# Optimization experiments

Measured on AMD Instinct MI355X. Metric: run time of the kernel, lower is better.

The kernel has to match this reference:

```python
import jax, jax.numpy as jnp
from jax import lax
import numpy as np

NEG = jnp.float32(-1e9)


def monotonic_alignment_search(logp, text_lengths, mel_lengths):
    """Glow-TTS style MAS. logp: [B, Tt, Tm] (log_softmax over text axis).
    Returns integer durations [B, Tt] summing to mel_lengths per batch."""
    B, Tt, Tm = logp.shape
    i_range = jnp.arange(Tt)
    text_mask = i_range[None, :] < text_lengths[:, None]            # [B, Tt]
    logp = jnp.where(text_mask[:, :, None], logp, NEG)

    # ---- forward DP over mel frames: Q[i,j] = logp[i,j] + max(Q[i,j-1], Q[i-1,j-1])
    q0 = jnp.where(i_range[None, :] == 0, logp[:, :, 0], NEG)        # [B, Tt]

    def fwd(q, lp_j):
        q_shift = jnp.concatenate([jnp.full((B, 1), NEG), q[:, :-1]], axis=1)
        take_diag = q_shift > q                                      # came from i-1
        q_new = lp_j + jnp.maximum(q, q_shift)
        return q_new, take_diag

    _, choices = lax.scan(fwd, q0, jnp.moveaxis(logp[:, :, 1:], 2, 0))  # [Tm-1, B, Tt]
    choices = jnp.concatenate([jnp.zeros((1, B, Tt), bool), choices], axis=0)  # align j

    # ---- backtrack from (text_len-1, mel_len-1) down to j=0
    b_idx = jnp.arange(B)

    def bwd(i, j):
        active = j < mel_lengths                                     # [B]
        dur_inc = (active[:, None] & (i_range[None, :] == i[:, None]))
        ch = choices[j, b_idx, i]                                    # [B] bool
        i_new = jnp.where(active & (j > 0), i - ch.astype(i.dtype), i)
        return i_new, dur_inc

    i0 = text_lengths - 1
    _, durs = lax.scan(bwd, i0, jnp.arange(Tm - 1, -1, -1))
    return durs.sum(0).astype(jnp.int32)                             # [B, Tt]


def length_regulate(h_text, durations, mel_lengths, Tm):
    """Expand h_text [B,Tt,D] by durations [B,Tt] to [B,Tm,D]."""
    B, Tt, D = h_text.shape
    cum = jnp.cumsum(durations, axis=1)                              # [B, Tt]
    j = jnp.arange(Tm)
    idx = (cum[:, None, :] <= j[None, :, None]).sum(-1)              # [B, Tm]
    idx = jnp.clip(idx, 0, Tt - 1)
    h_exp = jnp.take_along_axis(h_text, idx[:, :, None], axis=1)     # [B, Tm, D]
    mel_mask = j[None, :] < mel_lengths[:, None]
    return h_exp * mel_mask[:, :, None].astype(h_exp.dtype)


def setup_inputs() -> dict:
    B, Tt, Tm, D, M = 32, 512, 2048, 512, 80
    k = jax.random.split(jax.random.key(0), 6)
    return {
        "h_text": jax.random.normal(k[0], (B, Tt, D), jnp.float32),
        "mel": jax.random.normal(k[1], (B, M, Tm), jnp.float32),
        "text_lengths": jax.random.randint(k[2], (B,), 256, Tt + 1, jnp.int32),
        "mel_lengths": jax.random.randint(k[3], (B,), 1024, Tm + 1, jnp.int32),
        "w_proj": jax.random.normal(k[4], (D, M), jnp.float32) * 0.02,
        "b_proj": jnp.zeros((D,), jnp.float32),
        "log_dur_pred": jax.random.normal(k[5], (B, Tt), jnp.float32) * 0.5,
    }


def reference(h_text, mel, text_lengths, mel_lengths, w_proj, b_proj, log_dur_pred):
    B, Tt, D = h_text.shape
    Tm = mel.shape[2]

    # mel_proj = Linear(n_mels -> d_model) on mel.transpose(1,2)
    mel_proj = jnp.einsum('bmt,dm->btd', mel, w_proj) + b_proj       # [B, Tm, D]

    # alignment scores + masked log_softmax over text axis
    attn = jnp.einsum('btd,bsd->bts', h_text, mel_proj)              # [B, Tt, Tm]
    text_mask = jnp.arange(Tt)[None, :] >= text_lengths[:, None]
    mel_mask = jnp.arange(Tm)[None, :] >= mel_lengths[:, None]
    attn = jnp.where(text_mask[:, :, None], NEG, attn)
    attn = jnp.where(mel_mask[:, None, :], NEG, attn)
    logp = jax.nn.log_softmax(attn, axis=1)

    durations = monotonic_alignment_search(logp, text_lengths, mel_lengths)

    # duration loss (masked sum-MSE in log domain)
    dur_mask = (jnp.arange(Tt)[None, :] < text_lengths[:, None]).astype(jnp.float32)
    log_dur_gt = jnp.log(jnp.clip(durations.astype(jnp.float32), 1.0, None))
    diff = log_dur_pred * dur_mask - log_dur_gt * dur_mask
    dur_loss = jnp.sum(diff * diff) / jnp.sum(dur_mask)

    h_expanded = length_regulate(h_text, durations, mel_lengths, Tm)  # [B, Tm, D]
    return (h_expanded, dur_loss, durations)
```

## Files before the change

### kernel.cpp

```cpp
#include <hip/hip_runtime.h>
#include <math.h>

#define Bn 32
#define TT 512
#define TM 2048
#define DD 512
#define MMp 80
#define NEGF (-1.0e9f)

constexpr size_t LOSS_OFF = (size_t)Bn * TM * DD;
constexpr size_t DUR_OFF  = LOSS_OFF + 1;

__global__ __launch_bounds__(256) void k0_wtx(const float* __restrict__ w,
                                              const float* __restrict__ bias,
                                              float* __restrict__ wTx) {
    int m = blockIdx.x;
    for (int d = threadIdx.x; d < DD; d += 256) {
        float v = 0.f;
        if (m < 80) v = w[d * 80 + m];
        else if (m == 80) v = bias[d];
        wTx[m * DD + d] = v;
    }
}

__global__ __launch_bounds__(256) void k1_hw(const float* __restrict__ h_text,
                                             const float* __restrict__ wTx,
                                             float* __restrict__ hwX) {
    int bid = blockIdx.x;
    int b = bid >> 3;
    int i0 = (bid & 7) * 64;
    int t = threadIdx.x;
    int tr = t & 15, tc = t >> 4;
    __shared__ __align__(16) float Asub[64 * 68];
    __shared__ __align__(16) float Bsub[96 * 68];
    float acc[4][6];
#pragma unroll
    for (int a = 0; a < 4; ++a)
#pragma unroll
        for (int c = 0; c < 6; ++c) acc[a][c] = 0.f;

    for (int d0 = 0; d0 < DD; d0 += 64) {
        __syncthreads();
#pragma unroll
        for (int p = 0; p < 4; ++p) {
            int lin = p * 256 + t;
            int r = lin >> 4, dq = lin & 15;
            *(float4*)&Asub[r * 68 + dq * 4] =
                *(const float4*)&h_text[((size_t)(b * TT + i0 + r)) * DD + d0 + dq * 4];
        }
#pragma unroll
        for (int p = 0; p < 6; ++p) {
            int lin = p * 256 + t;
            int cc = lin >> 4, dq = lin & 15;
            *(float4*)&Bsub[cc * 68 + dq * 4] =
                *(const float4*)&wTx[(size_t)cc * DD + d0 + dq * 4];
        }
        __syncthreads();
#pragma unroll
        for (int dd = 0; dd < 16; ++dd) {
            float4 a[4], bb[6];
#pragma unroll
            for (int ri = 0; ri < 4; ++ri)
                a[ri] = *(const float4*)&Asub[(tr * 4 + ri) * 68 + dd * 4];
#pragma unroll
            for (int ci = 0; ci < 6; ++ci)
                bb[ci] = *(const float4*)&Bsub[(tc * 6 + ci) * 68 + dd * 4];
#pragma unroll
            for (int ri = 0; ri < 4; ++ri)
#pragma unroll
                for (int ci = 0; ci < 6; ++ci) {
                    acc[ri][ci] += a[ri].x * bb[ci].x;
                    acc[ri][ci] += a[ri].y * bb[ci].y;
                    acc[ri][ci] += a[ri].z * bb[ci].z;
                    acc[ri][ci] += a[ri].w * bb[ci].w;
                }
        }
    }
#pragma unroll
    for (int ri = 0; ri < 4; ++ri)
#pragma unroll
        for (int ci = 0; ci < 6; ++ci)
            hwX[((size_t)b * 96 + tc * 6 + ci) * DD + i0 + tr * 4 + ri] = acc[ri][ci];
}

__global__ __launch_bounds__(256) void k2_attn(const float* __restrict__ hwX,
                                               const float* __restrict__ mel,
                                               const int* __restrict__ tlen,
                                               const int* __restrict__ mlen,
                                               float* __restrict__ logpT) {
    const int b = blockIdx.y;
    const int ml = mlen[b];
    const int j0 = blockIdx.x * 32;
    if (j0 >= ml) return;
    const int tl = tlen[b];
    const int tid = threadIdx.x;
    const int ig = tid >> 2;
    const int jg = tid & 3;

    __shared__ __align__(16) float hwS[16 * 512];
    __shared__ __align__(16) float melS[16 * 32];
    __shared__ float red[32 * 64];
    __shared__ float colmax[32];
    __shared__ float lsum[32];

    float acc[8][8];
#pragma unroll
    for (int a = 0; a < 8; ++a)
#pragma unroll
        for (int c = 0; c < 8; ++c) acc[a][c] = 0.f;

    for (int mc = 0; mc < 80; mc += 16) {
        __syncthreads();
#pragma unroll
        for (int p = 0; p < 8; ++p) {
            int lin = p * 256 + tid;
            int mm = lin >> 7, iq = lin & 127;
            *(float4*)&hwS[mm * 512 + iq * 4] =
                *(const float4*)&hwX[((size_t)b * 96 + mc + mm) * DD + iq * 4];
        }
#pragma unroll
        for (int p = 0; p < 2; ++p) {
            int lin = p * 256 + tid;
            int mm = lin >> 5, jj = lin & 31;
            melS[lin] = mel[((size_t)b * 80 + mc + mm) * TM + j0 + jj];
        }
        __syncthreads();
#pragma unroll
        for (int mm = 0; mm < 16; ++mm) {
            float4 a0 = *(const float4*)&hwS[mm * 512 + ig * 8];
            float4 a1 = *(const float4*)&hwS[mm * 512 + ig * 8 + 4];
            float4 b0 = *(const float4*)&melS[mm * 32 + jg * 8];
            float4 b1 = *(const float4*)&melS[mm * 32 + jg * 8 + 4];
            float av[8] = {a0.x, a0.y, a0.z, a0.w, a1.x, a1.y, a1.z, a1.w};
            float bv[8] = {b0.x, b0.y, b0.z, b0.w, b1.x, b1.y, b1.z, b1.w};
#pragma unroll
            for (int ii = 0; ii < 8; ++ii)
#pragma unroll
                for (int jj = 0; jj < 8; ++jj) acc[ii][jj] += av[ii] * bv[jj];
        }
    }
    float4 h0 = *(const float4*)&hwX[((size_t)b * 96 + 80) * DD + ig * 8];
    float4 h1 = *(const float4*)&hwX[((size_t)b * 96 + 80) * DD + ig * 8 + 4];
    float hb[8] = {h0.x, h0.y, h0.z, h0.w, h1.x, h1.y, h1.z, h1.w};
#pragma unroll
    for (int ii = 0; ii < 8; ++ii) {
        bool valid = (ig * 8 + ii) < tl;
#pragma unroll
        for (int jj = 0; jj < 8; ++jj)
            acc[ii][jj] = valid ? (acc[ii][jj] + hb[ii]) : NEGF;
    }
    __syncthreads();
#pragma unroll
    for (int jj = 0; jj < 8; ++jj) {
        float m = acc[0][jj];
#pragma unroll
        for (int ii = 1; ii < 8; ++ii) m = fmaxf(m, acc[ii][jj]);
        red[(jg * 8 + jj) * 64 + ig] = m;
    }
    __syncthreads();
    if (tid < 32) {
        float m = red[tid * 64];
        for (int g = 1; g < 64; ++g) m = fmaxf(m, red[tid * 64 + g]);
        colmax[tid] = m;
    }
    __syncthreads();
#pragma unroll
    for (int jj = 0; jj < 8; ++jj) {
        float cm = colmax[jg * 8 + jj];
        float s = 0.f;
#pragma unroll
        for (int ii = 0; ii < 8; ++ii) s += expf(acc[ii][jj] - cm);
        red[(jg * 8 + jj) * 64 + ig] = s;
    }
    __syncthreads();
    if (tid < 32) {
        float s = 0.f;
        for (int g = 0; g < 64; ++g) s += red[tid * 64 + g];
        lsum[tid] = logf(s);
    }
    __syncthreads();
#pragma unroll
    for (int jj = 0; jj < 8; ++jj) {
        int j = j0 + jg * 8 + jj;
        if (j < ml) {
            float cm = colmax[jg * 8 + jj], ls = lsum[jg * 8 + jj];
            float o[8];
#pragma unroll
            for (int ii = 0; ii < 8; ++ii) {
                int i = ig * 8 + ii;
                o[ii] = (i < tl) ? ((acc[ii][jj] - cm) - ls) : NEGF;
            }
            float* dst = &logpT[((size_t)b * TM + j) * TT + ig * 8];
            *(float4*)dst = make_float4(o[0], o[1], o[2], o[3]);
            *(float4*)(dst + 4) = make_float4(o[4], o[5], o[6], o[7]);
        }
    }
}

#define KVB 16
#define NKB 128

typedef float vf4 __attribute__((ext_vector_type(4)));

__device__ __forceinline__ void lds_dma16(const float* g, float* l) {
    __builtin_amdgcn_global_load_lds((const __attribute__((address_space(1))) void*)g,
                                     (__attribute__((address_space(3))) void*)l,
                                     16, 0, 0);
}

#define SB0() __builtin_amdgcn_sched_barrier(0)

__device__ __forceinline__ float dpp_shr1(float old, float src) {
    return __int_as_float(__builtin_amdgcn_update_dpp(
        __float_as_int(old), __float_as_int(src), 0x138, 0xF, 0xF, false));
}
__device__ __forceinline__ float dpp_ror1(float src) {
    return __int_as_float(__builtin_amdgcn_update_dpp(
        __float_as_int(src), __float_as_int(src), 0x13C, 0xF, 0xF, false));
}

__global__ __launch_bounds__(64, 1) void k3_dp(const float* __restrict__ logpT,
                                               const int* __restrict__ tlen,
                                               const int* __restrict__ mlen,
                                               unsigned* __restrict__ gwords,
                                               int* __restrict__ idxmap,
                                               float* __restrict__ dOut) {
    const int b = blockIdx.x;
    const int lane = threadIdx.x;
    const int tl = tlen[b];
    const int ml = mlen[b];

    __shared__ __align__(16) float ring[2][KVB][512];
    __shared__ int durs[TT];
    for (int idx = lane; idx < TT; idx += 64) durs[idx] = 0;

    const float* colbase = logpT + (size_t)b * TM * TT;
    unsigned* gwb = gwords + (size_t)b * TT * 64;

    float qa[4], qb[4];
    unsigned accA[4], accB[4];
#pragma unroll
    for (int k = 0; k < 4; ++k) { qa[k] = NEGF; qb[k] = NEGF; accA[k] = 0u; accB[k] = 0u; }
    float q00 = colbase[0];
    asm volatile("" :: "v"(q00));
    if (lane == 0) qa[0] = q00;

    unsigned* gpA = gwb + (size_t)(4 * lane) * 64;
    unsigned* gpB = gwb + (size_t)(256 + 4 * lane) * 64;
    int woff = 0;
    int jj = 1;
    const int lane4 = lane * 4;

#define DMA_BATCH(nb_, slot_) do {                                             \
        const float* src_ = colbase + (size_t)(1 + (nb_) * KVB) * 512 + lane4; \
        float* dst_ = &ring[slot_][0][0];                                      \
        _Pragma("unroll")                                                      \
        for (int c_ = 0; c_ < KVB; ++c_) {                                     \
            lds_dma16(src_ + c_ * 512,       dst_ + c_ * 512);                 \
            lds_dma16(src_ + c_ * 512 + 256, dst_ + c_ * 512 + 256);           \
        }                                                                      \
    } while (0)

#define COL1(la_, lb_) do {                                                    \
        float wrap_ = dpp_ror1(qa[3]);                   \
        float nA0_ = dpp_shr1(NEGF, qa[3]);         \
        float nB0_ = dpp_shr1(wrap_, qb[3]);           \
        float nA_[4], nB_[4];                                                  \
        nA_[0] = nA0_; nB_[0] = nB0_;                                          \
        _Pragma("unroll")                                                      \
        for (int k_ = 1; k_ < 4; ++k_) { nA_[k_] = qa[k_ - 1]; nB_[k_] = qb[k_ - 1]; } \
        const unsigned m32_ = 1u << (jj & 31);                                 \
        _Pragma("unroll")                                                      \
        for (int k_ = 0; k_ < 4; ++k_) {                                       \
            if (nA_[k_] > qa[k_]) accA[k_] |= m32_;                            \
            qa[k_] = la_[k_] + fmaxf(qa[k_], nA_[k_]);                         \
            if (nB_[k_] > qb[k_]) accB[k_] |= m32_;                            \
            qb[k_] = lb_[k_] + fmaxf(qb[k_], nB_[k_]);                         \
        }                                                                      \
        if ((jj & 31) == 31) {                              \
            _Pragma("unroll")                                                  \
            for (int k_ = 0; k_ < 4; ++k_) {                                   \
                gpA[k_ * 64 + woff] = accA[k_]; accA[k_] = 0u;                 \
                gpB[k_ * 64 + woff] = accB[k_]; accB[k_] = 0u;                 \
            }                                                                  \
            ++woff;                                                            \
        }                                                                      \
        ++jj;                                                                  \
    } while (0)

#define READG(slab_, c0_, ga_, gb_) do {                                       \
        _Pragma("unroll")                                                      \
        for (int p_ = 0; p_ < 4; ++p_) {                                       \
            ga_[p_] = *(const vf4*)&slab_[(c0_ + p_) * 512 + lane4];           \
            gb_[p_] = *(const vf4*)&slab_[(c0_ + p_) * 512 + 256 + lane4];     \
        }                                                                      \
    } while (0)

#define COMPG(ga_, gb_) do {                                                   \
        _Pragma("unroll")                                                      \
        for (int p_ = 0; p_ < 4; ++p_) COL1(ga_[p_], gb_[p_]);                 \
    } while (0)

    DMA_BATCH(0, 0);
    DMA_BATCH(1, 1);

    for (int n = 0; n < NKB; ++n) {
        asm volatile("s_waitcnt vmcnt(32)" ::: "memory");
        SB0();
        const float* slab = &ring[n & 1][0][0];
        vf4 xA[4], xB[4], yA[4], yB[4];
        READG(slab, 0, xA, xB);
        READG(slab, 4, yA, yB);
        COMPG(xA, xB);
        READG(slab, 8, xA, xB);
        COMPG(yA, yB);
        READG(slab, 12, yA, yB);
        COMPG(xA, xB);
        COMPG(yA, yB);
        SB0();
        asm volatile("s_waitcnt lgkmcnt(0)" ::: "memory");
        SB0();
        if (n + 2 < NKB) DMA_BATCH(n + 2, n & 1);
        SB0();
    }
    asm volatile("s_waitcnt vmcnt(0) lgkmcnt(0)" ::: "memory");
#undef DMA_BATCH
#undef COL1
#undef READG
#undef COMPG

    __threadfence();
    __syncthreads();

    {
        int i = tl - 1;
        int j = ml - 1;
        unsigned r0, r1, r2, r3, r4, r5, r6, r7;
        {
            int a0 = tl - 1, a1 = tl - 2, a2 = tl - 3, a3 = tl - 4;
            int a4 = tl - 5, a5 = tl - 6, a6 = tl - 7, a7 = tl - 8;
            a1 = a1 < 0 ? 0 : a1; a2 = a2 < 0 ? 0 : a2; a3 = a3 < 0 ? 0 : a3;
            a4 = a4 < 0 ? 0 : a4; a5 = a5 < 0 ? 0 : a5; a6 = a6 < 0 ? 0 : a6;
            a7 = a7 < 0 ? 0 : a7;
            r0 = gwb[a0 * 64 + lane]; r1 = gwb[a1 * 64 + lane];
            r2 = gwb[a2 * 64 + lane]; r3 = gwb[a3 * 64 + lane];
            r4 = gwb[a4 * 64 + lane]; r5 = gwb[a5 * 64 + lane];
            r6 = gwb[a6 * 64 + lane]; r7 = gwb[a7 * 64 + lane];
        }
        int nf = tl - 9;
        int guard = TT + 2;
        while (guard-- > 0) {
            unsigned w = r0;
            r0 = r1; r1 = r2; r2 = r3; r3 = r4; r4 = r5; r5 = r6; r6 = r7;
            {
                int rf = (nf < 0) ? 0 : nf;
                r7 = gwb[rf * 64 + lane];
                --nf;
            }
            int jw = j >> 5, rr = j & 31;
            unsigned topmask = (rr == 31) ? 0xFFFFFFFFu : ((1u << (rr + 1)) - 1u);
            unsigned wm = (lane < jw) ? w : ((lane == jw) ? (w & topmask) : 0u);
            unsigned long long bal = __ballot(wm != 0u);
            if (bal == 0ull) {
                if (lane == 0) durs[i] = j + 1;
                break;
            }
            int hl = 63 - __clzll(bal);
            unsigned whl = (unsigned)__builtin_amdgcn_readlane((int)wm, hl);
            int jp = (hl << 5) + (31 - __clz(whl));
            if (lane == 0) durs[i] = j - jp + 1;
            j = jp - 1;
            if (--i < 0) break;
        }
    }
    __syncthreads();

    int d[8], pre[8];
    int run = 0;
#pragma unroll
    for (int k = 0; k < 8; ++k) { d[k] = durs[lane * 8 + k]; pre[k] = run; run += d[k]; }
    int v = run;
#pragma unroll
    for (int off = 1; off < 64; off <<= 1) {
        int n = __shfl_up(v, off);
        if (lane >= off) v += n;
    }
    int base = v - run;
#pragma unroll
    for (int k = 0; k < 8; ++k) {
        int i = lane * 8 + k;
        dOut[DUR_OFF + (size_t)b * TT + i] = (float)d[k];
        int st = base + pre[k];
        int en = st + d[k];
        if (en > TM) en = TM;
        if (st < 0) st = 0;
        for (int t2 = st; t2 < en; ++t2) idxmap[b * TM + t2] = i;
    }
}

__global__ __launch_bounds__(128) void k4_expand(const float* __restrict__ h_text,
                                                 const int* __restrict__ idxmap,
                                                 const int* __restrict__ mlen,
                                                 float* __restrict__ dOut) {
    int bid = blockIdx.x;
    int b = bid >> 11;
    int j = bid & (TM - 1);
    int t = threadIdx.x;
    float4* orow = (float4*)dOut + (size_t)bid * 128;
    if (j < mlen[b]) {
        int i = idxmap[bid] & (TT - 1);
        const float4* hrow = (const float4*)h_text + ((size_t)(b * TT + i)) * 128;
        orow[t] = hrow[t];
    } else {
        orow[t] = make_float4(0.f, 0.f, 0.f, 0.f);
    }
}

__global__ __launch_bounds__(256) void k5_loss(const float* __restrict__ pred,
                                               const int* __restrict__ tlen,
                                               float* __restrict__ dOut) {
    __shared__ float rs[256];
    __shared__ int rc[256];
    int t = threadIdx.x;
    float s = 0.f;
    int c = 0;
    for (int idx = t; idx < Bn * TT; idx += 256) {
        int b = idx >> 9, i = idx & 511;
        if (i < tlen[b]) {
            float dv = dOut[DUR_OFF + idx];
            float lg = logf(fmaxf(dv, 1.0f));
            float df = pred[idx] - lg;
            s += df * df;
            c += 1;
        }
    }
    rs[t] = s; rc[t] = c;
    __syncthreads();
    for (int off = 128; off > 0; off >>= 1) {
        if (t < off) { rs[t] += rs[t + off]; rc[t] += rc[t + off]; }
        __syncthreads();
    }
    if (t == 0) dOut[LOSS_OFF] = rs[0] / (float)rc[0];
}

extern "C" void kernel_launch(void* const* d_in, const int* in_sizes, int n_in,
                              void* d_out, int out_size, void* d_ws, size_t ws_size,
                              hipStream_t stream) {
    const float* h_text = (const float*)d_in[0];
    const float* mel    = (const float*)d_in[1];
    const int*   tlen   = (const int*)d_in[2];
    const int*   mlen   = (const int*)d_in[3];
    const float* w      = (const float*)d_in[4];
    const float* bias   = (const float*)d_in[5];
    const float* pred   = (const float*)d_in[6];
    float* out = (float*)d_out;

    float*    logpT  = (float*)d_ws;
    float*    hwX    = logpT + (size_t)Bn * TM * TT;
    float*    wTx    = hwX + (size_t)Bn * 96 * DD;
    unsigned* gwords = (unsigned*)(wTx + 96 * DD);
    int*      idxmap = (int*)(gwords + (size_t)Bn * TT * 64);

    k0_wtx<<<dim3(96), dim3(256), 0, stream>>>(w, bias, wTx);
    k1_hw<<<dim3(256), dim3(256), 0, stream>>>(h_text, wTx, hwX);
    k2_attn<<<dim3(64, 32), dim3(256), 0, stream>>>(hwX, mel, tlen, mlen, logpT);
    k3_dp<<<dim3(32), dim3(64), 0, stream>>>(logpT, tlen, mlen, gwords, idxmap, out);
    k4_expand<<<dim3(Bn * TM), dim3(128), 0, stream>>>(h_text, idxmap, mlen, out);
    k5_loss<<<dim3(1), dim3(256), 0, stream>>>(pred, tlen, out);
}
```

Baseline: 829.4 us.

## Split DP kernel into compute wave and eight producer DMA waves

The single-wave MAS forward DP kernel becomes a 576-thread block. Wave 0 runs the serial DP recurrence out of LDS, while eight producer waves each DMA two columns of the next 16-column batch into the other ring slot. Each batch ends with a __syncthreads instead of the old hand-tuned vmcnt waits. The aim is to take global-to-LDS load issue off the latency-critical DP wave, at the cost of a block barrier per batch and going from two batches of prefetch to one.

```diff
diff --git a/kernel.cpp b/kernel.cpp
--- a/kernel.cpp
+++ b/kernel.cpp
@@ -199,6 +199,7 @@
 
 #define KVB 16
 #define NKB 128
+#define K3T 576
 
 typedef float vf4 __attribute__((ext_vector_type(4)));
 
@@ -208,8 +209,6 @@
                                      16, 0, 0);
 }
 
-#define SB0() __builtin_amdgcn_sched_barrier(0)
-
 __device__ __forceinline__ float dpp_shr1(float old, float src) {
     return __int_as_float(__builtin_amdgcn_update_dpp(
         __float_as_int(old), __float_as_int(src), 0x138, 0xF, 0xF, false));
@@ -219,20 +218,22 @@
         __float_as_int(src), __float_as_int(src), 0x13C, 0xF, 0xF, false));
 }
 
-__global__ __launch_bounds__(64, 1) void k3_dp(const float* __restrict__ logpT,
-                                               const int* __restrict__ tlen,
-                                               const int* __restrict__ mlen,
-                                               unsigned* __restrict__ gwords,
-                                               int* __restrict__ idxmap,
-                                               float* __restrict__ dOut) {
+__global__ __launch_bounds__(K3T, 1) void k3_dp(const float* __restrict__ logpT,
+                                                const int* __restrict__ tlen,
+                                                const int* __restrict__ mlen,
+                                                unsigned* __restrict__ gwords,
+                                                int* __restrict__ idxmap,
+                                                float* __restrict__ dOut) {
     const int b = blockIdx.x;
-    const int lane = threadIdx.x;
+    const int tid = threadIdx.x;
+    const int wid = tid >> 6;
+    const int lane = tid & 63;
     const int tl = tlen[b];
     const int ml = mlen[b];
 
     __shared__ __align__(16) float ring[2][KVB][512];
     __shared__ int durs[TT];
-    for (int idx = lane; idx < TT; idx += 64) durs[idx] = 0;
+    for (int idx = tid; idx < TT; idx += K3T) durs[idx] = 0;
 
     const float* colbase = logpT + (size_t)b * TM * TT;
     unsigned* gwb = gwords + (size_t)b * TT * 64;
@@ -241,24 +242,23 @@
     unsigned accA[4], accB[4];
 #pragma unroll
     for (int k = 0; k < 4; ++k) { qa[k] = NEGF; qb[k] = NEGF; accA[k] = 0u; accB[k] = 0u; }
-    float q00 = colbase[0];
-    asm volatile("" :: "v"(q00));
-    if (lane == 0) qa[0] = q00;
-
+    if (wid == 0 && lane == 0) qa[0] = colbase[0];
     unsigned* gpA = gwb + (size_t)(4 * lane) * 64;
     unsigned* gpB = gwb + (size_t)(256 + 4 * lane) * 64;
     int woff = 0;
     int jj = 1;
     const int lane4 = lane * 4;
 
-#define DMA_BATCH(nb_, slot_) do {                                             \
-        const float* src_ = colbase + (size_t)(1 + (nb_) * KVB) * 512 + lane4; \
-        float* dst_ = &ring[slot_][0][0];                                      \
-        _Pragma("unroll")                                                      \
-        for (int c_ = 0; c_ < KVB; ++c_) {                                     \
-            lds_dma16(src_ + c_ * 512,       dst_ + c_ * 512);                 \
-            lds_dma16(src_ + c_ * 512 + 256, dst_ + c_ * 512 + 256);           \
-        }                                                                      \
+    const int pc0 = (wid - 1) * 2;
+
+#define DMA_2COLS(nb_, slot_) do {                                             \
+        const int j0_ = 1 + (nb_) * KVB + pc0;                                 \
+        const float* src_ = colbase + (size_t)j0_ * 512 + lane4;               \
+        float* dst_ = &ring[slot_][pc0][0];                                    \
+        lds_dma16(src_,             dst_);                                     \
+        lds_dma16(src_ + 256,       dst_ + 256);                               \
+        lds_dma16(src_ + 512,       dst_ + 512);                               \
+        lds_dma16(src_ + 512 + 256, dst_ + 512 + 256);                         \
     } while (0)
 
 #define COL1(la_, lb_) do {                                                    \
@@ -301,30 +301,27 @@
         for (int p_ = 0; p_ < 4; ++p_) COL1(ga_[p_], gb_[p_]);                 \
     } while (0)
 
-    DMA_BATCH(0, 0);
-    DMA_BATCH(1, 1);
+    if (wid > 0) DMA_2COLS(0, 0);
+    __syncthreads();
 
     for (int n = 0; n < NKB; ++n) {
-        asm volatile("s_waitcnt vmcnt(32)" ::: "memory");
-        SB0();
-        const float* slab = &ring[n & 1][0][0];
-        vf4 xA[4], xB[4], yA[4], yB[4];
-        READG(slab, 0, xA, xB);
-        READG(slab, 4, yA, yB);
-        COMPG(xA, xB);
-        READG(slab, 8, xA, xB);
-        COMPG(yA, yB);
-        READG(slab, 12, yA, yB);
-        COMPG(xA, xB);
-        COMPG(yA, yB);
-        SB0();
-        asm volatile("s_waitcnt lgkmcnt(0)" ::: "memory");
-        SB0();
-        if (n + 2 < NKB) DMA_BATCH(n + 2, n & 1);
-        SB0();
-    }
-    asm volatile("s_waitcnt vmcnt(0) lgkmcnt(0)" ::: "memory");
-#undef DMA_BATCH
+        if (wid == 0) {
+            const float* slab = &ring[n & 1][0][0];
+            vf4 xA[4], xB[4], yA[4], yB[4];
+            READG(slab, 0, xA, xB);
+            READG(slab, 4, yA, yB);
+            COMPG(xA, xB);
+            READG(slab, 8, xA, xB);
+            COMPG(yA, yB);
+            READG(slab, 12, yA, yB);
+            COMPG(xA, xB);
+            COMPG(yA, yB);
+        } else {
+            if (n + 1 < NKB) DMA_2COLS(n + 1, (n + 1) & 1);
+        }
+        __syncthreads();
+    }
+#undef DMA_2COLS
 #undef COL1
 #undef READG
 #undef COMPG
@@ -332,69 +329,70 @@
     __threadfence();
     __syncthreads();
 
-    {
-        int i = tl - 1;
-        int j = ml - 1;
-        unsigned r0, r1, r2, r3, r4, r5, r6, r7;
+    if (wid == 0) {
         {
-            int a0 = tl - 1, a1 = tl - 2, a2 = tl - 3, a3 = tl - 4;
-            int a4 = tl - 5, a5 = tl - 6, a6 = tl - 7, a7 = tl - 8;
-            a1 = a1 < 0 ? 0 : a1; a2 = a2 < 0 ? 0 : a2; a3 = a3 < 0 ? 0 : a3;
-            a4 = a4 < 0 ? 0 : a4; a5 = a5 < 0 ? 0 : a5; a6 = a6 < 0 ? 0 : a6;
-            a7 = a7 < 0 ? 0 : a7;
-            r0 = gwb[a0 * 64 + lane]; r1 = gwb[a1 * 64 + lane];
-            r2 = gwb[a2 * 64 + lane]; r3 = gwb[a3 * 64 + lane];
-            r4 = gwb[a4 * 64 + lane]; r5 = gwb[a5 * 64 + lane];
-            r6 = gwb[a6 * 64 + lane]; r7 = gwb[a7 * 64 + lane];
-        }
-        int nf = tl - 9;
-        int guard = TT + 2;
-        while (guard-- > 0) {
-            unsigned w = r0;
-            r0 = r1; r1 = r2; r2 = r3; r3 = r4; r4 = r5; r5 = r6; r6 = r7;
+            int i = tl - 1;
+            int j = ml - 1;
+            unsigned r0, r1, r2, r3, r4, r5, r6, r7;
             {
-                int rf = (nf < 0) ? 0 : nf;
-                r7 = gwb[rf * 64 + lane];
-                --nf;
+                int a0 = tl - 1, a1 = tl - 2, a2 = tl - 3, a3 = tl - 4;
+                int a4 = tl - 5, a5 = tl - 6, a6 = tl - 7, a7 = tl - 8;
+                a1 = a1 < 0 ? 0 : a1; a2 = a2 < 0 ? 0 : a2; a3 = a3 < 0 ? 0 : a3;
+                a4 = a4 < 0 ? 0 : a4; a5 = a5 < 0 ? 0 : a5; a6 = a6 < 0 ? 0 : a6;
+                a7 = a7 < 0 ? 0 : a7;
+                r0 = gwb[a0 * 64 + lane]; r1 = gwb[a1 * 64 + lane];
+                r2 = gwb[a2 * 64 + lane]; r3 = gwb[a3 * 64 + lane];
+                r4 = gwb[a4 * 64 + lane]; r5 = gwb[a5 * 64 + lane];
+                r6 = gwb[a6 * 64 + lane]; r7 = gwb[a7 * 64 + lane];
             }
-            int jw = j >> 5, rr = j & 31;
-            unsigned topmask = (rr == 31) ? 0xFFFFFFFFu : ((1u << (rr + 1)) - 1u);
-            unsigned wm = (lane < jw) ? w : ((lane == jw) ? (w & topmask) : 0u);
-            unsigned long long bal = __ballot(wm != 0u);
-            if (bal == 0ull) {
-                if (lane == 0) durs[i] = j + 1;
-                break;
+            int nf = tl - 9;
+            int guard = TT + 2;
+            while (guard-- > 0) {
+                unsigned w = r0;
+                r0 = r1; r1 = r2; r2 = r3; r3 = r4; r4 = r5; r5 = r6; r6 = r7;
+                {
+                    int rf = (nf < 0) ? 0 : nf;
+                    r7 = gwb[rf * 64 + lane];
+                    --nf;
+                }
+                int jw = j >> 5, rr = j & 31;
+                unsigned topmask = (rr == 31) ? 0xFFFFFFFFu : ((1u << (rr + 1)) - 1u);
+                unsigned wm = (lane < jw) ? w : ((lane == jw) ? (w & topmask) : 0u);
+                unsigned long long bal = __ballot(wm != 0u);
+                if (bal == 0ull) {
+                    if (lane == 0) durs[i] = j + 1;
+                    break;
+                }
+                int hl = 63 - __clzll(bal);
+                unsigned whl = (unsigned)__builtin_amdgcn_readlane((int)wm, hl);
+                int jp = (hl << 5) + (31 - __clz(whl));
+                if (lane == 0) durs[i] = j - jp + 1;
+                j = jp - 1;
+                if (--i < 0) break;
             }
-            int hl = 63 - __clzll(bal);
-            unsigned whl = (unsigned)__builtin_amdgcn_readlane((int)wm, hl);
-            int jp = (hl << 5) + (31 - __clz(whl));
-            if (lane == 0) durs[i] = j - jp + 1;
-            j = jp - 1;
-            if (--i < 0) break;
-        }
-    }
-    __syncthreads();
-
-    int d[8], pre[8];
-    int run = 0;
-#pragma unroll
-    for (int k = 0; k < 8; ++k) { d[k] = durs[lane * 8 + k]; pre[k] = run; run += d[k]; }
-    int v = run;
-#pragma unroll
-    for (int off = 1; off < 64; off <<= 1) {
-        int n = __shfl_up(v, off);
-        if (lane >= off) v += n;
-    }
-    int base = v - run;
-#pragma unroll
-    for (int k = 0; k < 8; ++k) {
-        int i = lane * 8 + k;
-        dOut[DUR_OFF + (size_t)b * TT + i] = (float)d[k];
-        int st = base + pre[k];
-        int en = st + d[k];
-        if (en > TM) en = TM;
-        if (st < 0) st = 0;
-        for (int t2 = st; t2 < en; ++t2) idxmap[b * TM + t2] = i;
+        }
+
+        int d[8], pre[8];
+        int run = 0;
+#pragma unroll
+        for (int k = 0; k < 8; ++k) { d[k] = durs[lane * 8 + k]; pre[k] = run; run += d[k]; }
+        int v = run;
+#pragma unroll
+        for (int off = 1; off < 64; off <<= 1) {
+            int n = __shfl_up(v, off);
+            if (lane >= off) v += n;
+        }
+        int base = v - run;
+#pragma unroll
+        for (int k = 0; k < 8; ++k) {
+            int i = lane * 8 + k;
+            dOut[DUR_OFF + (size_t)b * TT + i] = (float)d[k];
+            int st = base + pre[k];
+            int en = st + d[k];
+            if (en > TM) en = TM;
+            if (st < 0) st = 0;
+            for (int t2 = st; t2 < en; ++t2) idxmap[b * TM + t2] = i;
+        }
     }
 }
 
@@ -464,7 +462,7 @@
     k0_wtx<<<dim3(96), dim3(256), 0, stream>>>(w, bias, wTx);
     k1_hw<<<dim3(256), dim3(256), 0, stream>>>(h_text, wTx, hwX);
     k2_attn<<<dim3(64, 32), dim3(256), 0, stream>>>(hwX, mel, tlen, mlen, logpT);
-    k3_dp<<<dim3(32), dim3(64), 0, stream>>>(logpT, tlen, mlen, gwords, idxmap, out);
+    k3_dp<<<dim3(32), dim3(K3T), 0, stream>>>(logpT, tlen, mlen, gwords, idxmap, out);
     k4_expand<<<dim3(Bn * TM), dim3(128), 0, stream>>>(h_text, idxmap, mlen, out);
     k5_loss<<<dim3(1), dim3(256), 0, stream>>>(pred, tlen, out);
 }
```

New measurement: 843.0 us. About the same (+1.6%).
